# Performance work log

Hardware: AMD Instinct MI355X
Metric: run time of the kernel (lower is better)

Reference implementation:

```python
import math
import jax, jax.numpy as jnp
import numpy as np

SR = 44100.0
N_SAMPLES = 65536
BW_OCT = 1.0
F0_HZ = 440.0            # f0_min_hz == f0_max_hz -> fixed, no RNG
AM_HZ_MIN, AM_HZ_MAX = 4.0, 16.0
FM_OCT_HZ_MIN, FM_OCT_HZ_MAX = 0.5, 4.0
SIGMA0 = 0.1
BW_N_SAMPLES = int(BW_OCT * SR)   # 44100
LN2 = math.log(2.0)


def setup_inputs() -> dict:
    key = jax.random.key(0)
    k1, k2, k3 = jax.random.split(key, 3)
    B = 256
    theta_am_hz_0to1 = jax.random.uniform(k1, (B,), dtype=jnp.float32)
    theta_fm_hz_0to1 = jax.random.uniform(k2, (B,), dtype=jnp.float32)
    seed = jax.random.randint(k3, (B,), 0, 100000).astype(jnp.int64)
    return {"theta_am_hz_0to1": theta_am_hz_0to1,
            "theta_fm_hz_0to1": theta_fm_hz_0to1,
            "seed": seed}


def _synth(theta_am_hz_0to1, theta_fm_hz_0to1):
    # map [0,1] -> log2-uniform in [min,max]
    am_lo, am_hi = math.log2(AM_HZ_MIN), math.log2(AM_HZ_MAX)
    fm_lo, fm_hi = math.log2(FM_OCT_HZ_MIN), math.log2(FM_OCT_HZ_MAX)
    am_hz = jnp.exp2(theta_am_hz_0to1 * (am_hi - am_lo) + am_lo)      # [B]
    fm_hz = jnp.exp2(theta_fm_hz_0to1 * (fm_hi - fm_lo) + fm_lo)      # [B]

    # time support and gaussian-window support (both [N])
    t = (jnp.arange(N_SAMPLES, dtype=jnp.float32) - N_SAMPLES // 2) / SR
    half = (N_SAMPLES - 1) / 2.0
    win_support = jnp.linspace(-half, half, N_SAMPLES, dtype=jnp.float32)

    fm = fm_hz[:, None]                                               # [B,1]
    am = am_hz[:, None]                                               # [B,1]
    two_pi = 2.0 * jnp.pi

    # FM chirp phase: f0/(fm*ln2) * (2^(fm*t) - 1)
    phi = (F0_HZ / (fm * LN2)) * (jnp.exp2(fm * t) - 1.0)             # [B,N]
    carrier = jnp.sin(two_pi * phi)
    modulator = jnp.sin(two_pi * am * 0.5 * t)

    # gaussian window, std = |sigma0 * bw_n_samples / fm| (per sample)
    window_std = jnp.abs(SIGMA0 * BW_N_SAMPLES / fm)                  # [B,1]
    w = win_support * (1.0 / (window_std * math.sqrt(2.0)))
    window = jnp.exp(-(w * w))                                        # [B,N]

    chirp = carrier * fm * window * modulator                         # fm!=0, am>0
    return chirp[:, None, :]                                          # [B,1,N]


def reference(theta_am_hz_0to1, theta_fm_hz_0to1, seed):
    # seed is unused: f0_min==f0_max and delta_min==delta_max==0, so the
    # per-sample torch RNG in the original is never consulted.
    return _synth(theta_am_hz_0to1, theta_fm_hz_0to1)
```

## Files before the change

kernel.cpp:

```cpp
#include <hip/hip_runtime.h>

#define NS 65536
#define CHUNK_LOG 4
#define CHUNK_SAMPLES 4096

typedef float f32x4 __attribute__((ext_vector_type(4)));

__global__ __launch_bounds__(256) void chirplet_synth_kernel(
    const float* __restrict__ theta_am,
    const float* __restrict__ theta_fm,
    float* __restrict__ out)
{
    const int bid   = blockIdx.x;
    const int b     = bid >> CHUNK_LOG;
    const int chunk = bid & ((1 << CHUNK_LOG) - 1);
    const int base  = chunk * CHUNK_SAMPLES;

    const float tf = theta_fm[b];
    const float fm = exp2f(tf * 3.0f - 1.0f);

    float* outp = out + (size_t)b * NS + base + (threadIdx.x << 2);

    const float T  = 31182.0f / fm;
    const float lo = (float)base - 32767.5f;
    const float hi = (float)(base + CHUNK_SAMPLES - 1) - 32767.5f;
    if (lo > T || hi < -T) {
        const f32x4 z = {0.f, 0.f, 0.f, 0.f};
#pragma unroll
        for (int j = 0; j < 4; ++j)
            __builtin_nontemporal_store(z, reinterpret_cast<f32x4*>(outp + (j << 10)));
        return;
    }

    const float ta      = theta_am[b];
    const float am      = exp2f(ta * 2.0f + 2.0f);
    const float c       = 440.0f / (fm * 0.69314718055994531f);
    const float inv_den = fm * (1.0f / 6236.68503f);
    const float am_half = am * 0.5f;
    const float inv_sr  = 1.0f / 44100.0f;
    const float LOG2E   = 1.44269504088896340f;

#pragma unroll
    for (int j = 0; j < 4; ++j) {
        const int n0 = base + (threadIdx.x << 2) + (j << 10);
        float res[4];
#pragma unroll
        for (int i = 0; i < 4; ++i) {
            const float nf = (float)(n0 + i);
            const float t  = (nf - 32768.0f) * inv_sr;
            const float ws = nf - 32767.5f;

            const float e    = exp2f(fm * t);
            const float phi  = c * (e - 1.0f);
            const float carr = __builtin_amdgcn_sinf(__builtin_amdgcn_fractf(phi));
            const float modu = __builtin_amdgcn_sinf(__builtin_amdgcn_fractf(am_half * t));

            const float wv  = ws * inv_den;
            const float win = exp2f(-(wv * wv) * LOG2E);

            res[i] = carr * fm * win * modu;
        }
        f32x4 r = {res[0], res[1], res[2], res[3]};
        __builtin_nontemporal_store(r, reinterpret_cast<f32x4*>(outp + (j << 10)));
    }
}

extern "C" void kernel_launch(void* const* d_in, const int* in_sizes, int n_in,
                              void* d_out, int out_size, void* d_ws, size_t ws_size,
                              hipStream_t stream) {
    const float* theta_am = (const float*)d_in[0];
    const float* theta_fm = (const float*)d_in[1];
    float* out = (float*)d_out;

    const int B = in_sizes[0];
    dim3 grid(B << CHUNK_LOG), block(256);
    chirplet_synth_kernel<<<grid, block, 0, stream>>>(theta_am, theta_fm, out);
}
```

Baseline: 88.04 us.

## Replace per-sample transcendentals with recurrences and skip zero-window groups

Computes the exponential chirp term, Gaussian window and AM modulator incrementally, using multiplicative and rotation recurrences across the four samples per thread and across 1024-sample groups. This replaces several exp2/sin calls per sample with multiplies and FMAs. Groups whose window exponent underflows are written as zeros without doing the math. Each block now covers twice as many samples with half as many blocks. The recurrences may drift numerically, and the larger chunks mean fewer blocks.

Result: faster. 81.89 us (-7.0%).

```diff
diff --git a/kernel.cpp b/kernel.cpp
--- a/kernel.cpp
+++ b/kernel.cpp
@@ -1,8 +1,9 @@
 #include <hip/hip_runtime.h>
 
 #define NS 65536
-#define CHUNK_LOG 4
-#define CHUNK_SAMPLES 4096
+#define CHUNK_LOG 3
+#define GROUPS 8
+#define CHUNK_SAMPLES (GROUPS * 1024)
 
 typedef float f32x4 __attribute__((ext_vector_type(4)));
 
@@ -15,53 +16,87 @@
     const int b     = bid >> CHUNK_LOG;
     const int chunk = bid & ((1 << CHUNK_LOG) - 1);
     const int base  = chunk * CHUNK_SAMPLES;
+    const int tid4  = threadIdx.x << 2;
 
     const float tf = theta_fm[b];
     const float fm = exp2f(tf * 3.0f - 1.0f);
 
-    float* outp = out + (size_t)b * NS + base + (threadIdx.x << 2);
+    float* outp = out + (size_t)b * NS + base + tid4;
 
-    const float T  = 31182.0f / fm;
-    const float lo = (float)base - 32767.5f;
-    const float hi = (float)(base + CHUNK_SAMPLES - 1) - 32767.5f;
-    if (lo > T || hi < -T) {
-        const f32x4 z = {0.f, 0.f, 0.f, 0.f};
+    const float T = 31182.0f / fm;
+    {
+        const float lo = (float)base - 32767.5f;
+        const float hi = (float)(base + CHUNK_SAMPLES - 1) - 32767.5f;
+        if (lo > T || hi < -T) {
+            const f32x4 z = {0.f, 0.f, 0.f, 0.f};
 #pragma unroll
-        for (int j = 0; j < 4; ++j)
-            __builtin_nontemporal_store(z, reinterpret_cast<f32x4*>(outp + (j << 10)));
-        return;
+            for (int gi = 0; gi < GROUPS; ++gi)
+                __builtin_nontemporal_store(z, reinterpret_cast<f32x4*>(outp + (gi << 10)));
+            return;
+        }
     }
 
-    const float ta      = theta_am[b];
-    const float am      = exp2f(ta * 2.0f + 2.0f);
-    const float c       = 440.0f / (fm * 0.69314718055994531f);
-    const float inv_den = fm * (1.0f / 6236.68503f);
-    const float am_half = am * 0.5f;
-    const float inv_sr  = 1.0f / 44100.0f;
-    const float LOG2E   = 1.44269504088896340f;
+    const float ta = theta_am[b];
+    const float am = exp2f(ta * 2.0f + 2.0f);
+
+    const float inv_sr = 1.0f / 44100.0f;
+    const float n0f = (float)(base + tid4);
+    const float t0  = (n0f - 32768.0f) * inv_sr;
+    const float ws0 = n0f - 32767.5f;
+
+    const float c  = 440.0f / (fm * 0.69314718055994531f);
+    const float r1 = exp2f(fm * inv_sr);
+
+    const float invd = fm * (1.0f / 6236.68503f);
+    const float k2   = invd * invd * 1.44269504f;
+    const float P1   = exp2f(-2.0f * k2);
+
+    const float m1  = am * (0.5f * inv_sr);
+    const float th0 = am * 0.5f * t0;
+    float s  = __builtin_amdgcn_sinf(__builtin_amdgcn_fractf(th0));
+    float cc = __builtin_amdgcn_cosf(__builtin_amdgcn_fractf(th0));
+    const float sd1 = __builtin_amdgcn_sinf(m1);
+    const float cd1 = __builtin_amdgcn_cosf(m1);
+    const float mG  = m1 * 1024.0f;
+    const float sdG = __builtin_amdgcn_sinf(__builtin_amdgcn_fractf(mG));
+    const float cdG = __builtin_amdgcn_cosf(__builtin_amdgcn_fractf(mG));
 
 #pragma unroll
-    for (int j = 0; j < 4; ++j) {
-        const int n0 = base + (threadIdx.x << 2) + (j << 10);
-        float res[4];
+    for (int gi = 0; gi < GROUPS; ++gi) {
+        const float ws_g = ws0 + (float)(gi << 10);
+        const float q    = -k2 * ws_g * ws_g;
+
+        if (q > -36.5f) {
+            const float t_g = (n0f + (float)(gi << 10) - 32768.0f) * inv_sr;
+            float e  = exp2f(fm * t_g);
+            float g  = fm * exp2f(q);
+            float v1 = exp2f(-k2 * (2.0f * ws_g + 1.0f));
+            float ls = s, lc = cc;
+
+            float res[4];
 #pragma unroll
-        for (int i = 0; i < 4; ++i) {
-            const float nf = (float)(n0 + i);
-            const float t  = (nf - 32768.0f) * inv_sr;
-            const float ws = nf - 32767.5f;
+            for (int i = 0; i < 4; ++i) {
+                const float phi  = c * (e - 1.0f);
+                const float carr = __builtin_amdgcn_sinf(__builtin_amdgcn_fractf(phi));
+                res[i] = carr * g * ls;
+                if (i < 3) {
+                    e *= r1;
+                    g *= v1;  v1 *= P1;
+                    const float ns = __builtin_fmaf(ls, cd1,  lc * sd1);
+                    const float nc = __builtin_fmaf(lc, cd1, -ls * sd1);
+                    ls = ns; lc = nc;
+                }
+            }
+            f32x4 r = {res[0], res[1], res[2], res[3]};
+            __builtin_nontemporal_store(r, reinterpret_cast<f32x4*>(outp + (gi << 10)));
+        } else {
+            const f32x4 z = {0.f, 0.f, 0.f, 0.f};
+            __builtin_nontemporal_store(z, reinterpret_cast<f32x4*>(outp + (gi << 10)));
+        }
 
-            const float e    = exp2f(fm * t);
-            const float phi  = c * (e - 1.0f);
-            const float carr = __builtin_amdgcn_sinf(__builtin_amdgcn_fractf(phi));
-            const float modu = __builtin_amdgcn_sinf(__builtin_amdgcn_fractf(am_half * t));
-
-            const float wv  = ws * inv_den;
-            const float win = exp2f(-(wv * wv) * LOG2E);
-
-            res[i] = carr * fm * win * modu;
-        }
-        f32x4 r = {res[0], res[1], res[2], res[3]};
-        __builtin_nontemporal_store(r, reinterpret_cast<f32x4*>(outp + (j << 10)));
+        const float ns = __builtin_fmaf(s, cdG,  cc * sdG);
+        const float nc = __builtin_fmaf(cc, cdG, -s * sdG);
+        s = ns; cc = nc;
     }
 }
 
```
